# Performance work log

Measured on AMD Instinct MI355X. Metric: run time of the kernel, lower is better.

## Reference

```python
import jax, jax.numpy as jnp
import numpy as np

N, D = 1_000_000, 128
B, S1, S2 = 4096, 25, 10
M = B * (1 + S2)  # layer-2 frontier: batch nodes + their sampled neighbors


def setup_inputs() -> dict:
    key = jax.random.key(0)
    k1, k2, k3, k4, k5, k6 = jax.random.split(key, 6)
    Z = jax.random.normal(k1, (N, D), dtype=jnp.float32)
    W1 = jax.random.normal(k2, (D, 2 * D), dtype=jnp.float32) * 0.05
    W2 = jax.random.normal(k3, (D, 2 * D), dtype=jnp.float32) * 0.05
    node_idx = jax.random.randint(k4, (M,), 0, N, dtype=jnp.int32)
    nbr1 = jax.random.randint(k5, (M, S1), 0, N, dtype=jnp.int32)
    nbr2 = jax.random.randint(k6, (B, S2), 0, M, dtype=jnp.int32)
    return {"Z": Z, "W1": W1, "W2": W2, "node_idx": node_idx,
            "nbr1": nbr1, "nbr2": nbr2}


def _sage_layer(h_self, h_nbr_mean, W):
    # z = sigmoid(W @ cat([h_v, mean(h_u)])); then L2-normalize
    z = jax.nn.sigmoid(jnp.concatenate([h_self, h_nbr_mean], axis=-1) @ W.T)
    return z * jax.lax.rsqrt(jnp.sum(z * z, axis=-1, keepdims=True))


def reference(Z, W1, W2, node_idx, nbr1, nbr2):
    # Layer 1: compute updated embeddings for all M frontier nodes
    h_self = Z[node_idx]                 # [M, D] gather
    h_nbr = Z[nbr1].mean(axis=1)         # [M, S1, D] gather -> mean -> [M, D]
    h1 = _sage_layer(h_self, h_nbr, W1)  # [M, D]
    # Layer 2: batch nodes are the first B entries of the frontier
    h2_nbr = h1[nbr2].mean(axis=1)       # [B, D]
    h2 = _sage_layer(h1[:B], h2_nbr, W2)  # [B, D]
    return h2
```

## Files before the change

kernel.cpp:

```cpp
#include <hip/hip_runtime.h>
#include <hip/hip_bf16.h>
#include <cstdint>

#define NN 1000000
#define DD 128
#define BB 4096
#define S1C 25
#define S2C 10
#define MM 45056

using f32x4 = __attribute__((ext_vector_type(4))) float;
using s16x8 = __attribute__((ext_vector_type(8))) short;

__device__ __forceinline__ ushort f2bf(float x) {
    uint32_t u = __float_as_uint(x);
    u += 0x7fff + ((u >> 16) & 1);
    return (ushort)(u >> 16);
}
__device__ __forceinline__ float bf2f(ushort h) {
    return __uint_as_float(((uint32_t)h) << 16);
}

__global__ __launch_bounds__(256) void k_gather1(
    const float* __restrict__ Z, const int* __restrict__ node_idx,
    const int* __restrict__ nbr1, ushort* __restrict__ cat1)
{
    const int lane = threadIdx.x & 63;
    const int half = lane >> 5;
    const int c    = lane & 31;
    const int m = blockIdx.x * 4 + (threadIdx.x >> 6);

    const int nbv  = nbr1[(size_t)m * S1C + (lane < S1C ? lane : S1C - 1)];
    const int self = node_idx[m];

    f32x4 acc = {0.f, 0.f, 0.f, 0.f};
    #pragma unroll
    for (int j = 0; j < 12; ++j) {
        const int idx = __shfl(nbv, 2 * j + half, 64);
        const f32x4 v = *(const f32x4*)(Z + (size_t)idx * DD + c * 4);
        acc.x += v.x; acc.y += v.y; acc.z += v.z; acc.w += v.w;
    }
    const int idx24 = __shfl(nbv, S1C - 1, 64);
    const int base  = half ? idx24 : self;
    const f32x4 vs  = *(const f32x4*)(Z + (size_t)base * DD + c * 4);
    if (half) { acc.x += vs.x; acc.y += vs.y; acc.z += vs.z; acc.w += vs.w; }

    f32x4 tot;
    tot.x = acc.x + __shfl_xor(acc.x, 32, 64);
    tot.y = acc.y + __shfl_xor(acc.y, 32, 64);
    tot.z = acc.z + __shfl_xor(acc.z, 32, 64);
    tot.w = acc.w + __shfl_xor(acc.w, 32, 64);

    if (half == 0) {
        const float inv = 1.0f / S1C;
        ushort4 os, om;
        os.x = f2bf(vs.x);        os.y = f2bf(vs.y);
        os.z = f2bf(vs.z);        os.w = f2bf(vs.w);
        om.x = f2bf(tot.x * inv); om.y = f2bf(tot.y * inv);
        om.z = f2bf(tot.z * inv); om.w = f2bf(tot.w * inv);
        ushort* crow = cat1 + (size_t)m * 256;
        *(ushort4*)(crow + c * 4)       = os;
        *(ushort4*)(crow + 128 + c * 4) = om;
    }
}

__global__ __launch_bounds__(256) void k_gather2(
    const ushort* __restrict__ h1, const int* __restrict__ nbr2,
    ushort* __restrict__ cat2)
{
    const int lane = threadIdx.x & 63;
    const int half = lane >> 5;
    const int c    = lane & 31;
    const int b = blockIdx.x * 4 + (threadIdx.x >> 6);

    const int nbv = nbr2[(size_t)b * S2C + (lane < S2C ? lane : S2C - 1)];

    float a0 = 0.f, a1 = 0.f, a2 = 0.f, a3 = 0.f;
    #pragma unroll
    for (int j = 0; j < 5; ++j) {
        const int idx = __shfl(nbv, 2 * j + half, 64);
        const uint2 v = *(const uint2*)(h1 + (size_t)idx * DD + c * 4);
        a0 += bf2f((ushort)(v.x & 0xffffu));
        a1 += bf2f((ushort)(v.x >> 16));
        a2 += bf2f((ushort)(v.y & 0xffffu));
        a3 += bf2f((ushort)(v.y >> 16));
    }
    const uint2 sv = *(const uint2*)(h1 + (size_t)b * DD + c * 4);

    float t0 = a0 + __shfl_xor(a0, 32, 64);
    float t1 = a1 + __shfl_xor(a1, 32, 64);
    float t2 = a2 + __shfl_xor(a2, 32, 64);
    float t3 = a3 + __shfl_xor(a3, 32, 64);

    if (half == 0) {
        const float inv = 1.0f / S2C;
        ushort4 om;
        om.x = f2bf(t0 * inv); om.y = f2bf(t1 * inv);
        om.z = f2bf(t2 * inv); om.w = f2bf(t3 * inv);
        ushort* crow = cat2 + (size_t)b * 256;
        *(uint2*)(crow + c * 4)           = sv;
        *(ushort4*)(crow + 128 + c * 4)   = om;
    }
}

template<int OUT_BF16>
__global__ __launch_bounds__(256) void k_sage(
    const ushort* __restrict__ cat, const float* __restrict__ W,
    void* __restrict__ out)
{
    __shared__ ushort Wl[128][256];
    const int tid = threadIdx.x;
    #pragma unroll
    for (int it = 0; it < 32; ++it) {
        int i = it * 256 + tid;
        float4 w = ((const float4*)W)[i];
        int e = i << 2;
        int r = e >> 8, c = e & 255;
        int cs = c ^ ((r & 7) << 3);
        ushort4 o;
        o.x = f2bf(w.x); o.y = f2bf(w.y); o.z = f2bf(w.z); o.w = f2bf(w.w);
        *(ushort4*)&Wl[r][cs] = o;
    }
    __syncthreads();

    const int lane = tid & 63;
    const int q = lane >> 4;
    const int p = lane & 15;
    const int row0 = blockIdx.x * 64 + (tid >> 6) * 16;

    const ushort* arow = cat + (size_t)(row0 + p) * 256 + q * 8;
    f32x4 acc[8] = {};
    #pragma unroll
    for (int ks = 0; ks < 8; ++ks) {
        s16x8 a = *(const s16x8*)(arow + ks * 32);
        #pragma unroll
        for (int t = 0; t < 8; ++t) {
            const int d = t * 16 + p;
            const int kcol = (ks * 32 + q * 8) ^ ((d & 7) << 3);
            s16x8 b = *(const s16x8*)&Wl[d][kcol];
            acc[t] = __builtin_amdgcn_mfma_f32_16x16x32_bf16(a, b, acc[t], 0, 0, 0);
        }
    }

    float z[8][4];
    float ss[4] = {0.f, 0.f, 0.f, 0.f};
    #pragma unroll
    for (int t = 0; t < 8; ++t)
        #pragma unroll
        for (int r = 0; r < 4; ++r) {
            float v = 1.0f / (1.0f + __expf(-acc[t][r]));
            z[t][r] = v;
            ss[r] += v * v;
        }
    #pragma unroll
    for (int r = 0; r < 4; ++r) {
        float s = ss[r];
        s += __shfl_xor(s, 1);
        s += __shfl_xor(s, 2);
        s += __shfl_xor(s, 4);
        s += __shfl_xor(s, 8);
        ss[r] = rsqrtf(s);
    }
    #pragma unroll
    for (int t = 0; t < 8; ++t)
        #pragma unroll
        for (int r = 0; r < 4; ++r) {
            int row = row0 + q * 4 + r;
            int col = t * 16 + p;
            float v = z[t][r] * ss[r];
            if (OUT_BF16) ((ushort*)out)[(size_t)row * DD + col] = f2bf(v);
            else          ((float*)out)[(size_t)row * DD + col]  = v;
        }
}

extern "C" void kernel_launch(void* const* d_in, const int* in_sizes, int n_in,
                              void* d_out, int out_size, void* d_ws, size_t ws_size,
                              hipStream_t stream)
{
    const float* Z        = (const float*)d_in[0];
    const float* W1       = (const float*)d_in[1];
    const float* W2       = (const float*)d_in[2];
    const int*   node_idx = (const int*)d_in[3];
    const int*   nbr1     = (const int*)d_in[4];
    const int*   nbr2     = (const int*)d_in[5];

    ushort* cat1 = (ushort*)d_ws;
    ushort* h1   = cat1 + (size_t)MM * 256;
    ushort* cat2 = h1   + (size_t)MM * DD;

    k_gather1<<<MM / 4, 256, 0, stream>>>(Z, node_idx, nbr1, cat1);
    k_sage<1><<<MM / 64, 256, 0, stream>>>(cat1, W1, (void*)h1);
    k_gather2<<<BB / 4, 256, 0, stream>>>(h1, nbr2, cat2);
    k_sage<0><<<BB / 64, 256, 0, stream>>>(cat2, W2, d_out);
}
```

Before: 678.5 us.

## Pre-convert Z to bf16 table and gather bf16 rows in layer-1

Adds a kernel that converts the whole fp32 embedding table Z to bf16 in workspace, then layer-1 gather reads the 256-byte bf16 rows instead of 512-byte fp32 rows, with four quarter-waves each loading 16-byte chunks. The intent is to halve the bytes moved by the random-access gather. The cost is a full streaming pass over the 512 MB Z table, reading it and writing 256 MB, on every call. That pass is far larger than the roughly 600 MB the gather touches, so it likely outweighs the savings.

Result: slower. 771.6 us (+13.7%).

```diff
diff --git a/kernel.cpp b/kernel.cpp
--- a/kernel.cpp
+++ b/kernel.cpp
@@ -9,8 +9,9 @@
 #define S2C 10
 #define MM 45056
 
-using f32x4 = __attribute__((ext_vector_type(4))) float;
-using s16x8 = __attribute__((ext_vector_type(8))) short;
+using f32x4  = __attribute__((ext_vector_type(4))) float;
+using s16x8  = __attribute__((ext_vector_type(8))) short;
+using u16x8  = __attribute__((ext_vector_type(8))) unsigned short;
 
 __device__ __forceinline__ ushort f2bf(float x) {
     uint32_t u = __float_as_uint(x);
@@ -21,46 +22,63 @@
     return __uint_as_float(((uint32_t)h) << 16);
 }
 
+__global__ __launch_bounds__(256) void k_conv(
+    const float* __restrict__ Z, ushort* __restrict__ Zb)
+{
+    const size_t stride = (size_t)2048 * 256;
+    const size_t G = (size_t)NN * DD / 8;
+    for (size_t g = (size_t)blockIdx.x * 256 + threadIdx.x; g < G; g += stride) {
+        f32x4 a = ((const f32x4*)Z)[g * 2];
+        f32x4 b = ((const f32x4*)Z)[g * 2 + 1];
+        u16x8 o;
+        o[0] = f2bf(a.x); o[1] = f2bf(a.y); o[2] = f2bf(a.z); o[3] = f2bf(a.w);
+        o[4] = f2bf(b.x); o[5] = f2bf(b.y); o[6] = f2bf(b.z); o[7] = f2bf(b.w);
+        ((u16x8*)Zb)[g] = o;
+    }
+}
+
 __global__ __launch_bounds__(256) void k_gather1(
-    const float* __restrict__ Z, const int* __restrict__ node_idx,
+    const ushort* __restrict__ Zb, const int* __restrict__ node_idx,
     const int* __restrict__ nbr1, ushort* __restrict__ cat1)
 {
     const int lane = threadIdx.x & 63;
-    const int half = lane >> 5;
-    const int c    = lane & 31;
+    const int qt   = lane >> 4;
+    const int c16  = lane & 15;
     const int m = blockIdx.x * 4 + (threadIdx.x >> 6);
 
     const int nbv  = nbr1[(size_t)m * S1C + (lane < S1C ? lane : S1C - 1)];
     const int self = node_idx[m];
 
-    f32x4 acc = {0.f, 0.f, 0.f, 0.f};
-    #pragma unroll
-    for (int j = 0; j < 12; ++j) {
-        const int idx = __shfl(nbv, 2 * j + half, 64);
-        const f32x4 v = *(const f32x4*)(Z + (size_t)idx * DD + c * 4);
-        acc.x += v.x; acc.y += v.y; acc.z += v.z; acc.w += v.w;
+    float facc[8] = {};
+    #pragma unroll
+    for (int j = 0; j < 6; ++j) {
+        const int idx = __shfl(nbv, 4 * j + qt, 64);
+        const u16x8 d = *(const u16x8*)(Zb + (size_t)idx * DD + c16 * 8);
+        #pragma unroll
+        for (int e = 0; e < 8; ++e) facc[e] += bf2f(d[e]);
     }
     const int idx24 = __shfl(nbv, S1C - 1, 64);
-    const int base  = half ? idx24 : self;
-    const f32x4 vs  = *(const f32x4*)(Z + (size_t)base * DD + c * 4);
-    if (half) { acc.x += vs.x; acc.y += vs.y; acc.z += vs.z; acc.w += vs.w; }
-
-    f32x4 tot;
-    tot.x = acc.x + __shfl_xor(acc.x, 32, 64);
-    tot.y = acc.y + __shfl_xor(acc.y, 32, 64);
-    tot.z = acc.z + __shfl_xor(acc.z, 32, 64);
-    tot.w = acc.w + __shfl_xor(acc.w, 32, 64);
-
-    if (half == 0) {
+    const int base7 = (qt == 0) ? self : idx24;
+    const u16x8 d7  = *(const u16x8*)(Zb + (size_t)base7 * DD + c16 * 8);
+    if (qt == 1) {
+        #pragma unroll
+        for (int e = 0; e < 8; ++e) facc[e] += bf2f(d7[e]);
+    }
+
+    #pragma unroll
+    for (int e = 0; e < 8; ++e) {
+        facc[e] += __shfl_xor(facc[e], 16, 64);
+        facc[e] += __shfl_xor(facc[e], 32, 64);
+    }
+
+    if (qt == 0) {
         const float inv = 1.0f / S1C;
-        ushort4 os, om;
-        os.x = f2bf(vs.x);        os.y = f2bf(vs.y);
-        os.z = f2bf(vs.z);        os.w = f2bf(vs.w);
-        om.x = f2bf(tot.x * inv); om.y = f2bf(tot.y * inv);
-        om.z = f2bf(tot.z * inv); om.w = f2bf(tot.w * inv);
+        u16x8 mv;
+        #pragma unroll
+        for (int e = 0; e < 8; ++e) mv[e] = f2bf(facc[e] * inv);
         ushort* crow = cat1 + (size_t)m * 256;
-        *(ushort4*)(crow + c * 4)       = os;
-        *(ushort4*)(crow + 128 + c * 4) = om;
+        *(u16x8*)(crow + c16 * 8)       = d7;
+        *(u16x8*)(crow + 128 + c16 * 8) = mv;
     }
 }
 
@@ -184,11 +202,13 @@
     const int*   nbr1     = (const int*)d_in[4];
     const int*   nbr2     = (const int*)d_in[5];
 
-    ushort* cat1 = (ushort*)d_ws;
+    ushort* Zb   = (ushort*)d_ws;
+    ushort* cat1 = Zb   + (size_t)NN * DD;
     ushort* h1   = cat1 + (size_t)MM * 256;
     ushort* cat2 = h1   + (size_t)MM * DD;
 
-    k_gather1<<<MM / 4, 256, 0, stream>>>(Z, node_idx, nbr1, cat1);
+    k_conv<<<2048, 256, 0, stream>>>(Z, Zb);
+    k_gather1<<<MM / 4, 256, 0, stream>>>(Zb, node_idx, nbr1, cat1);
     k_sage<1><<<MM / 64, 256, 0, stream>>>(cat1, W1, (void*)h1);
     k_gather2<<<BB / 4, 256, 0, stream>>>(h1, nbr2, cat2);
     k_sage<0><<<BB / 64, 256, 0, stream>>>(cat2, W2, d_out);
```
